# Kernel tuning notes

Hardware: AMD Instinct MI355X
Metric: run time of the kernel (lower is better)

The kernel has to match this reference:

```python
import jax, jax.numpy as jnp
import numpy as np

B, S, HID = 2, 2048, 2048
NH, NKV, HD = 16, 8, 256
EPS = 1e-6
SCALE = 256 ** -0.5  # query_pre_attn_scalar ** -0.5


def setup_inputs() -> dict:
    key = jax.random.key(0)
    k1, k2, k3 = jax.random.split(key, 3)
    hidden_states = jax.random.normal(k1, (B, S, HID), dtype=jnp.float32)
    w_qkv = jax.random.normal(k2, (HID, (NH + 2 * NKV) * HD), dtype=jnp.float32) * 0.02
    w_o = jax.random.normal(k3, (NH * HD, HID), dtype=jnp.float32) * 0.02
    q_norm_w = jnp.zeros((HD,), dtype=jnp.float32)  # Gemma RMSNorm uses (1 + w)
    k_norm_w = jnp.zeros((HD,), dtype=jnp.float32)
    # Real rotary tables: inv_freq over half dim, emb = concat(freqs, freqs)
    inv_freq = 1.0 / (10000.0 ** (jnp.arange(0, HD, 2, dtype=jnp.float32) / HD))
    pos = jnp.arange(S, dtype=jnp.float32)
    freqs = pos[:, None] * inv_freq[None, :]            # [S, HD/2]
    emb = jnp.concatenate([freqs, freqs], axis=-1)       # [S, HD]
    cos = jnp.broadcast_to(jnp.cos(emb)[None], (B, S, HD))
    sin = jnp.broadcast_to(jnp.sin(emb)[None], (B, S, HD))
    return {"hidden_states": hidden_states, "cos": cos, "sin": sin,
            "w_qkv": w_qkv, "w_o": w_o, "q_norm_w": q_norm_w, "k_norm_w": k_norm_w}


def _rms_norm(x, w):
    # Gemma3RMSNorm: fp32 rms, scale by (1 + w)
    xf = x.astype(jnp.float32)
    var = jnp.mean(xf * xf, axis=-1, keepdims=True)
    out = xf * jax.lax.rsqrt(var + EPS) * (1.0 + w.astype(jnp.float32))
    return out.astype(x.dtype)


def _rotate_half(x):
    x1, x2 = jnp.split(x, 2, axis=-1)
    return jnp.concatenate([-x2, x1], axis=-1)


def reference(hidden_states, cos, sin, w_qkv, w_o, q_norm_w, k_norm_w):
    qkv = jnp.einsum("bsh,hf->bsf", hidden_states, w_qkv)
    q, k, v = jnp.split(qkv, [NH * HD, NH * HD + NKV * HD], axis=-1)
    q = q.reshape(B, S, NH, HD).transpose(0, 2, 1, 3)    # [b, nh, s, d]
    k = k.reshape(B, S, NKV, HD).transpose(0, 2, 1, 3)   # [b, nkv, s, d]
    v = v.reshape(B, S, NKV, HD).transpose(0, 2, 1, 3)
    q = _rms_norm(q, q_norm_w)
    k = _rms_norm(k, k_norm_w)
    c = cos[:, None, :, :]  # broadcast over heads
    s = sin[:, None, :, :]
    q = q * c + _rotate_half(q) * s
    k = k * c + _rotate_half(k) * s
    n_rep = NH // NKV
    k = jnp.repeat(k, n_rep, axis=1)  # GQA expand: [b, nh, s, d]
    v = jnp.repeat(v, n_rep, axis=1)
    scores = jnp.einsum("bhqd,bhkd->bhqk", q, k) * SCALE
    attn = jax.nn.softmax(scores, axis=-1)
    out = jnp.einsum("bhqk,bhkd->bhqd", attn, v)
    out = out.transpose(0, 2, 1, 3).reshape(B, S, NH * HD)
    return jnp.einsum("bsf,fh->bsh", out, w_o)
```

## Files before the change

kernel.cpp:

```cpp
#include <hip/hip_runtime.h>
#include <stdint.h>

typedef __attribute__((ext_vector_type(8))) short short8;
typedef __attribute__((ext_vector_type(4))) short short4v;
typedef __attribute__((ext_vector_type(4))) float f32x4;

#define GLOAD16(gp, lp) __builtin_amdgcn_global_load_lds( \
    (__attribute__((address_space(1))) void*)(gp),        \
    (__attribute__((address_space(3))) void*)(lp), 16, 0, 0)

#define BAR   __builtin_amdgcn_s_barrier()
#define LGKM0 asm volatile("s_waitcnt lgkmcnt(0)" ::: "memory")
#define VMCNT4 asm volatile("s_waitcnt vmcnt(4)" ::: "memory")

__device__ __forceinline__ unsigned short f2bf(float f) {
    union { float f; unsigned u; } v; v.f = f;
    unsigned u = v.u + 0x7fffu + ((v.u >> 16) & 1u);
    return (unsigned short)(u >> 16);
}
__device__ __forceinline__ float bf2f(short s) {
    union { unsigned u; float f; } v;
    v.u = ((unsigned)(unsigned short)s) << 16;
    return v.f;
}

__global__ __launch_bounds__(256) void cvt_f32_bf16(const float* __restrict__ in,
                                                    short* __restrict__ out) {
    const int i = (blockIdx.x * 256 + threadIdx.x) * 4;
    const float4 v = *(const float4*)(in + i);
    short4v o;
    o[0] = (short)f2bf(v.x); o[1] = (short)f2bf(v.y);
    o[2] = (short)f2bf(v.z); o[3] = (short)f2bf(v.w);
    *(short4v*)(out + i) = o;
}

__global__ __launch_bounds__(256) void transpose_cvt(const float* __restrict__ in,
                                                     short* __restrict__ out,
                                                     int R, int C) {
    __shared__ float tile[64 * 65];
    const int t = threadIdx.x;
    const int r0 = blockIdx.y * 64, c0 = blockIdx.x * 64;
    const int rl = t >> 4, cl4 = (t & 15) * 4;
#pragma unroll
    for (int rep = 0; rep < 4; rep++) {
        const int r = rep * 16 + rl;
        const float4 v = *(const float4*)(in + (long)(r0 + r) * C + c0 + cl4);
        tile[r * 65 + cl4 + 0] = v.x;
        tile[r * 65 + cl4 + 1] = v.y;
        tile[r * 65 + cl4 + 2] = v.z;
        tile[r * 65 + cl4 + 3] = v.w;
    }
    __syncthreads();
#pragma unroll
    for (int rep = 0; rep < 4; rep++) {
        const int cc = rep * 16 + rl;
        short4v o;
#pragma unroll
        for (int j = 0; j < 4; j++) o[j] = (short)f2bf(tile[(cl4 + j) * 65 + cc]);
        *(short4v*)(out + (long)(c0 + cc) * R + r0 + cl4) = o;
    }
}

__global__ __launch_bounds__(256) void vtrans(const short* __restrict__ QKV,
                                              short* __restrict__ Vt) {
    __shared__ short tile[64 * 72];
    const int t = threadIdx.x;
    const int s0 = blockIdx.x * 64, d0 = blockIdx.y * 64;
    const int hb = blockIdx.z >> 1, b = blockIdx.z & 1;
    const short* src = QKV + ((long)(24 + hb) * 4096 + b * 2048) * 256;
    short* dst = Vt + (long)blockIdx.z * 256 * 2048;
#pragma unroll
    for (int p = 0; p < 2; p++) {
        const int c = p * 256 + t;
        const int r = c >> 3, col8 = (c & 7) * 8;
        *(short8*)(tile + r * 72 + col8) = *(const short8*)(src + (long)(s0 + r) * 256 + d0 + col8);
    }
    __syncthreads();
#pragma unroll
    for (int p = 0; p < 2; p++) {
        const int c = p * 256 + t;
        const int dr = c >> 3, sc8 = (c & 7) * 8;
        short8 o;
#pragma unroll
        for (int j = 0; j < 8; j++) o[j] = tile[(sc8 + j) * 72 + dr];
        *(short8*)(dst + (long)(d0 + dr) * 2048 + s0 + sc8) = o;
    }
}

template<int N, int K, int OUTMODE>
__global__ __launch_bounds__(256) void gemm_nt(const short* __restrict__ A,
                                               const short* __restrict__ Bt,
                                               void* __restrict__ Cv) {
    __shared__ __align__(16) short Al[128 * 32];
    __shared__ __align__(16) short Bl[128 * 32];
    const int t = threadIdx.x;
    const int lane = t & 63, w = t >> 6;
    const int quad = lane >> 4, l16 = lane & 15;
    const int wr = w >> 1, wc = w & 1;
    const long m0 = (long)blockIdx.y * 128, n0 = (long)blockIdx.x * 128;

    const short* Ag0 = A + (m0 + (t >> 2)) * K + (t & 3) * 8;
    const short* Bg0 = Bt + (n0 + (t >> 2)) * K + (t & 3) * 8;

    f32x4 acc[4][4] = {};

    for (int k0 = 0; k0 < K; k0 += 32) {
        __syncthreads();
        GLOAD16(Ag0 + k0,            Al + t * 8);
        GLOAD16(Ag0 + 64 * K + k0,   Al + (t + 256) * 8);
        GLOAD16(Bg0 + k0,            Bl + t * 8);
        GLOAD16(Bg0 + 64 * K + k0,   Bl + (t + 256) * 8);
        __syncthreads();
        short8 af[4], bfr[4];
#pragma unroll
        for (int i = 0; i < 4; i++)
            af[i] = *(const short8*)(Al + (wr * 64 + i * 16 + l16) * 32 + quad * 8);
#pragma unroll
        for (int i = 0; i < 4; i++)
            bfr[i] = *(const short8*)(Bl + (wc * 64 + i * 16 + l16) * 32 + quad * 8);
#pragma unroll
        for (int mi = 0; mi < 4; mi++)
#pragma unroll
            for (int ni = 0; ni < 4; ni++)
                acc[mi][ni] = __builtin_amdgcn_mfma_f32_16x16x32_bf16(af[mi], bfr[ni], acc[mi][ni], 0, 0, 0);
    }

    const long crow = m0 + wr * 64 + quad * 4;
    const long ccol = n0 + wc * 64 + l16;
    if constexpr (OUTMODE == 0) {
        float* C = (float*)Cv;
#pragma unroll
        for (int mi = 0; mi < 4; mi++)
#pragma unroll
            for (int ni = 0; ni < 4; ni++)
#pragma unroll
                for (int r = 0; r < 4; r++)
                    C[(crow + mi * 16 + r) * N + ccol + ni * 16] = acc[mi][ni][r];
    } else {
        short* C = (short*)Cv;
#pragma unroll
        for (int mi = 0; mi < 4; mi++)
#pragma unroll
            for (int ni = 0; ni < 4; ni++)
#pragma unroll
                for (int r = 0; r < 4; r++) {
                    const long m = crow + mi * 16 + r;
                    const long f = ccol + ni * 16;
                    C[(f >> 8) * 1048576 + m * 256 + (f & 255)] = (short)f2bf(acc[mi][ni][r]);
                }
    }
}

__global__ __launch_bounds__(512, 2) void gemm256_qkv(const short* __restrict__ A,
                                                      const short* __restrict__ Bt,
                                                      short* __restrict__ QKV) {
    constexpr int K = 2048;
    constexpr int NTM = 31;
    __shared__ __align__(16) short L[2][4][8192];

    const int t = threadIdx.x;
    const int lane = t & 63, w = t >> 6;
    const int quad = lane >> 4, l16 = lane & 15;
    const int wr = w >> 2, wc = w & 3;
    const int bh = 2 + (wc >> 1);
    const int brow0 = (wc & 1) * 64;

    const int flat = blockIdx.y * 32 + blockIdx.x;
    const int swz = (flat & 7) * 64 + (flat >> 3);
    const int bx = swz & 31, by = swz >> 5;
    const long m0 = (long)by * 256, n0 = (long)bx * 256;

    const int r0 = t >> 3, r1 = (512 + t) >> 3;
    const int k0s = ((t & 7) * 8) ^ (((r0 >> 2) & 1) << 4);
    const int k1s = ((t & 7) * 8) ^ (((r1 >> 2) & 1) << 4);
    const short* aS0 = A + (m0 + r0) * K + k0s;
    const short* aS1 = A + (m0 + r1) * K + k1s;
    const short* aT0 = aS0 + 128 * K;
    const short* aT1 = aS1 + 128 * K;
    const short* bS0 = Bt + (n0 + r0) * K + k0s;
    const short* bS1 = Bt + (n0 + r1) * K + k1s;
    const short* bT0 = bS0 + 128 * K;
    const short* bT1 = bS1 + 128 * K;

#define STG(p0, p1, bsel, slot, kt) do {                     \
    const int _ko = ((kt) & NTM) * 64;                       \
    GLOAD16((p0) + _ko, &L[bsel][slot][t * 8]);              \
    GLOAD16((p1) + _ko, &L[bsel][slot][4096 + t * 8]);       \
} while (0)

#define LDA4(bsel, rb) do {                                                        \
    _Pragma("unroll") for (int m = 0; m < 4; ++m) {                                \
        const int _r = (rb) + m * 16 + l16;                                        \
        const int _sw = ((_r >> 2) & 1) << 4;                                      \
        a[m][0] = *(const short8*)(&L[bsel][wr][_r * 64 + ((quad * 8) ^ _sw)]);    \
        a[m][1] = *(const short8*)(&L[bsel][wr][_r * 64 + ((32 + quad * 8) ^ _sw)]); \
    } } while (0)

#define LDB2(bsel, nb) do {                                                        \
    _Pragma("unroll") for (int n = 0; n < 2; ++n) {                                \
        const int _r = brow0 + ((nb) + n) * 16 + l16;                              \
        const int _sw = ((_r >> 2) & 1) << 4;                                      \
        b[(nb) + n][0] = *(const short8*)(&L[bsel][bh][_r * 64 + ((quad * 8) ^ _sw)]); \
        b[(nb) + n][1] = *(const short8*)(&L[bsel][bh][_r * 64 + ((32 + quad * 8) ^ _sw)]); \
    } } while (0)

#define PH_MFMA(MB, NB)                                                            \
    __builtin_amdgcn_s_setprio(1);                                                 \
    _Pragma("unroll") for (int m = 0; m < 4; ++m)                                  \
    _Pragma("unroll") for (int n = 0; n < 2; ++n)                                  \
    _Pragma("unroll") for (int kk = 0; kk < 2; ++kk)                               \
        acc[(MB) + m][(NB) + n] = __builtin_amdgcn_mfma_f32_16x16x32_bf16(         \
            a[m][kk], b[(NB) + n][kk], acc[(MB) + m][(NB) + n], 0, 0, 0);          \
    __builtin_amdgcn_s_setprio(0);

    short8 a[4][2], b[4][2];
    f32x4 acc[8][4] = {};

    STG(aS0, aS1, 0, 0, 0);
    STG(aT0, aT1, 0, 1, 0);
    STG(bS0, bS1, 0, 2, 0);
    STG(bT0, bT1, 0, 3, 0);
    STG(bS0, bS1, 1, 2, 1);
    STG(bT0, bT1, 1, 3, 1);
    VMCNT4;
    BAR;

    for (int it = 0; it < 16; ++it) {
        const int kt0 = 2 * it;
        LDA4(0, 0);
        LDB2(0, 0);
        STG(aS0, aS1, 1, 0, kt0 + 1);
        BAR; LGKM0;
        PH_MFMA(0, 0);
        BAR;
        LDB2(0, 2);
        STG(aT0, aT1, 1, 1, kt0 + 1);
        BAR; LGKM0;
        PH_MFMA(0, 2);
        BAR;
        LDA4(0, 64);
        STG(bS0, bS1, 0, 2, kt0 + 2);
        BAR; LGKM0;
        PH_MFMA(4, 2);
        BAR;
        STG(bT0, bT1, 0, 3, kt0 + 2);
        BAR;
        PH_MFMA(4, 0);
        VMCNT4;
        BAR;
        LDA4(1, 0);
        LDB2(1, 0);
        STG(aS0, aS1, 0, 0, kt0 + 2);
        BAR; LGKM0;
        PH_MFMA(0, 0);
        BAR;
        LDB2(1, 2);
        STG(aT0, aT1, 0, 1, kt0 + 2);
        BAR; LGKM0;
        PH_MFMA(0, 2);
        BAR;
        LDA4(1, 64);
        STG(bS0, bS1, 1, 2, kt0 + 3);
        BAR; LGKM0;
        PH_MFMA(4, 2);
        BAR;
        STG(bT0, bT1, 1, 3, kt0 + 3);
        BAR;
        PH_MFMA(4, 0);
        VMCNT4;
        BAR;
    }

    short* Cp = QKV + (long)bx * 1048576;
    const int cbase = wc * 64;
#pragma unroll
    for (int mi = 0; mi < 8; ++mi)
#pragma unroll
        for (int ni = 0; ni < 4; ++ni)
#pragma unroll
            for (int r = 0; r < 4; ++r) {
                const long m = m0 + wr * 128 + mi * 16 + quad * 4 + r;
                Cp[m * 256 + cbase + ni * 16 + l16] = (short)f2bf(acc[mi][ni][r]);
            }

#undef STG
#undef LDA4
#undef LDB2
#undef PH_MFMA
}

__global__ __launch_bounds__(256) void prep_qk(short* __restrict__ QKV,
                                               const float* __restrict__ cosp,
                                               const float* __restrict__ sinp,
                                               const float* __restrict__ qw,
                                               const float* __restrict__ kw) {
    const int t = threadIdx.x, w = t >> 6, lane = t & 63;
    const int d4 = lane * 4;
    const float sgn = (lane < 32) ? -1.0f : 1.0f;
#pragma unroll
    for (int i = 0; i < 4; i++) {
        const int g = blockIdx.x * 16 + w * 4 + i;
        const int u = g >> 12, m = g & 4095;
        short* rowp = QKV + (long)g * 256;
        const short4v raw = *(const short4v*)(rowp + d4);
        float x[4];
#pragma unroll
        for (int j = 0; j < 4; j++) x[j] = bf2f(raw[j]);
        float ss = x[0]*x[0] + x[1]*x[1] + x[2]*x[2] + x[3]*x[3];
#pragma unroll
        for (int msk = 1; msk < 64; msk <<= 1) ss += __shfl_xor(ss, msk, 64);
        const float rinv = rsqrtf(ss * (1.0f / 256.0f) + 1e-6f);
        const float4 wv = *(const float4*)(((u < 16) ? qw : kw) + d4);
        const float wa[4] = {wv.x, wv.y, wv.z, wv.w};
        const float4 cv = *(const float4*)(cosp + (long)m * 256 + d4);
        const float4 sv = *(const float4*)(sinp + (long)m * 256 + d4);
        const float ca[4] = {cv.x, cv.y, cv.z, cv.w};
        const float sa[4] = {sv.x, sv.y, sv.z, sv.w};
        float n[4];
#pragma unroll
        for (int j = 0; j < 4; j++) n[j] = x[j] * rinv * (1.0f + wa[j]);
        const float scale = (u < 16) ? 0.0625f : 1.0f;
        short4v ov;
#pragma unroll
        for (int j = 0; j < 4; j++) {
            const float p = __shfl_xor(n[j], 32, 64);
            ov[j] = (short)f2bf((n[j] * ca[j] + sgn * p * sa[j]) * scale);
        }
        *(short4v*)(rowp + d4) = ov;
    }
}

__global__ __launch_bounds__(512, 2) void attn(const short* __restrict__ QKV,
                                               const short* __restrict__ Vt,
                                               short* __restrict__ O) {
    __shared__ __align__(16) short Kl[2][64 * 256];
    __shared__ __align__(16) short Vl[256 * 64];
    __shared__ __align__(16) short Pl[128 * 72];
    __shared__ __align__(16) float Ll[128];

    const int t = threadIdx.x, w = t >> 6, lane = t & 63;
    const int quad = lane >> 4, l16 = lane & 15;
    const int q0 = blockIdx.x * 128, h = blockIdx.y, b = blockIdx.z;
    const int kh = h >> 1;
    const short* Qp = QKV + ((long)h * 4096 + b * 2048 + q0) * 256;
    const short* Kp = QKV + ((long)(16 + kh) * 4096 + b * 2048) * 256;
    const short* Vp = Vt + (long)(kh * 2 + b) * 256 * 2048;

    short8 qf[8];
#pragma unroll
    for (int ks = 0; ks < 8; ks++)
        qf[ks] = *(const short8*)(Qp + (w * 16 + l16) * 256 + ks * 32 + quad * 8);

    f32x4 acc[4][4] = {};
    float li_[4] = {0.0f, 0.0f, 0.0f, 0.0f};

    const int qh = w >> 2, dstr = (w & 3) * 64;

#pragma unroll
    for (int i = 0; i < 4; i++) {
        const int c = i * 512 + t;
        const int rK = c >> 5, j = c & 31;
        GLOAD16(Kp + (long)rK * 256 + (j ^ (rK & 31)) * 8, Kl[0] + c * 8);
    }

    for (int kt = 0; kt < 32; kt++) {
        const int k0 = kt * 64;
        __syncthreads();

#pragma unroll
        for (int i = 0; i < 4; i++) {
            const int c = i * 512 + t;
            const int dV = c >> 3, j = c & 7;
            GLOAD16(Vp + (long)dV * 2048 + k0 + (j ^ (dV & 7)) * 8, Vl + c * 8);
        }
        const int kn = ((kt + 1) & 31) * 64;
#pragma unroll
        for (int i = 0; i < 4; i++) {
            const int c = i * 512 + t;
            const int rK = c >> 5, j = c & 31;
            GLOAD16(Kp + (long)(kn + rK) * 256 + (j ^ (rK & 31)) * 8, Kl[(kt + 1) & 1] + c * 8);
        }

        const short* Kb = Kl[kt & 1];
        f32x4 sc[4] = {};
#pragma unroll
        for (int ct = 0; ct < 4; ct++) {
            const int rowK = ct * 16 + l16;
#pragma unroll
            for (int ks = 0; ks < 8; ks++) {
                const int dc = (ks * 4 + quad) ^ (rowK & 31);
                const short8 kf = *(const short8*)(Kb + rowK * 256 + dc * 8);
                sc[ct] = __builtin_amdgcn_mfma_f32_16x16x32_bf16(qf[ks], kf, sc[ct], 0, 0, 0);
            }
        }

#pragma unroll
        for (int ct = 0; ct < 4; ct++) {
#pragma unroll
            for (int r = 0; r < 4; r++) {
                const float p = __expf(sc[ct][r]);
                li_[r] += p;
                Pl[(w * 16 + quad * 4 + r) * 72 + ct * 16 + l16] = (short)f2bf(p);
            }
        }
        __syncthreads();

#pragma unroll
        for (int k2 = 0; k2 < 2; k2++) {
            short8 pf[4];
#pragma unroll
            for (int mi2 = 0; mi2 < 4; mi2++)
                pf[mi2] = *(const short8*)(Pl + (qh * 64 + mi2 * 16 + l16) * 72 + k2 * 32 + quad * 8);
#pragma unroll
            for (int ni = 0; ni < 4; ni++) {
                const int dV = dstr + ni * 16 + l16;
                const int dc = (k2 * 4 + quad) ^ (dV & 7);
                const short8 vf = *(const short8*)(Vl + dV * 64 + dc * 8);
#pragma unroll
                for (int mi2 = 0; mi2 < 4; mi2++)
                    acc[mi2][ni] = __builtin_amdgcn_mfma_f32_16x16x32_bf16(pf[mi2], vf, acc[mi2][ni], 0, 0, 0);
            }
        }
    }

#pragma unroll
    for (int r = 0; r < 4; r++) {
        float v = li_[r];
        v += __shfl_xor(v, 1, 64);
        v += __shfl_xor(v, 2, 64);
        v += __shfl_xor(v, 4, 64);
        v += __shfl_xor(v, 8, 64);
        if (l16 == 0) Ll[w * 16 + quad * 4 + r] = v;
    }
    __syncthreads();

    short* Op = O + (long)(b * 2048 + q0 + qh * 64) * 4096 + h * 256 + dstr;
#pragma unroll
    for (int mi2 = 0; mi2 < 4; mi2++) {
        const float4 lv = *(const float4*)(Ll + qh * 64 + mi2 * 16 + quad * 4);
        const float inv[4] = {1.0f / lv.x, 1.0f / lv.y, 1.0f / lv.z, 1.0f / lv.w};
#pragma unroll
        for (int ni = 0; ni < 4; ni++)
#pragma unroll
            for (int r = 0; r < 4; r++)
                Op[(long)(mi2 * 16 + quad * 4 + r) * 4096 + ni * 16 + l16] =
                    (short)f2bf(acc[mi2][ni][r] * inv[r]);
    }
}

extern "C" void kernel_launch(void* const* d_in, const int* in_sizes, int n_in,
                              void* d_out, int out_size, void* d_ws, size_t ws_size,
                              hipStream_t stream) {
    const float* hs   = (const float*)d_in[0];
    const float* cosp = (const float*)d_in[1];
    const float* sinp = (const float*)d_in[2];
    const float* wqkv = (const float*)d_in[3];
    const float* wo   = (const float*)d_in[4];
    const float* qnw  = (const float*)d_in[5];
    const float* knw  = (const float*)d_in[6];
    float* out = (float*)d_out;

    short* poolA  = (short*)d_ws;
    short* Xb     = poolA;
    short* Wqkv_t = poolA + (size_t)4096 * 2048;
    short* QKV    = poolA + (size_t)4096 * 2048 + (size_t)8192 * 2048;
    short* Vt     = poolA;
    short* Ob     = poolA + (size_t)16 * 256 * 2048;
    short* Wo_t   = QKV;

    cvt_f32_bf16<<<8192, 256, 0, stream>>>(hs, Xb);
    transpose_cvt<<<dim3(128, 32), 256, 0, stream>>>(wqkv, Wqkv_t, 2048, 8192);
    gemm256_qkv<<<dim3(32, 16), 512, 0, stream>>>(Xb, Wqkv_t, QKV);
    prep_qk<<<6144, 256, 0, stream>>>(QKV, cosp, sinp, qnw, knw);
    vtrans<<<dim3(32, 4, 16), 256, 0, stream>>>(QKV, Vt);
    attn<<<dim3(16, 16, 2), 512, 0, stream>>>(QKV, Vt, Ob);
    transpose_cvt<<<dim3(32, 64), 256, 0, stream>>>(wo, Wo_t, 4096, 2048);
    gemm_nt<2048, 4096, 0><<<dim3(16, 32), 256, 0, stream>>>(Ob, Wo_t, (void*)out);
}
```

Before: 608.3 us.

## Retile attention QK^T into 32x32 warp tiles with swizzled P buffer and priority hints

Each wave now computes a 32x32 block of scores, with two query sub-tiles sharing each K fragment, instead of 16x64. This halves the K LDS reads per MFMA. The P scratch buffer drops its padding in favour of an XOR swizzle, which saves LDS while avoiding bank conflicts. s_setprio is raised around the MFMA sections. Row sums are now split across two waves, so extra barriers are needed to combine them in LDS, and each wave holds twice the Q fragment registers.

```diff
diff --git a/kernel.cpp b/kernel.cpp
--- a/kernel.cpp
+++ b/kernel.cpp
@@ -335,7 +335,7 @@
                                                short* __restrict__ O) {
     __shared__ __align__(16) short Kl[2][64 * 256];
     __shared__ __align__(16) short Vl[256 * 64];
-    __shared__ __align__(16) short Pl[128 * 72];
+    __shared__ __align__(16) short Pl[128 * 64];
     __shared__ __align__(16) float Ll[128];
 
     const int t = threadIdx.x, w = t >> 6, lane = t & 63;
@@ -346,13 +346,16 @@
     const short* Kp = QKV + ((long)(16 + kh) * 4096 + b * 2048) * 256;
     const short* Vp = Vt + (long)(kh * 2 + b) * 256 * 2048;
 
-    short8 qf[8];
-#pragma unroll
-    for (int ks = 0; ks < 8; ks++)
-        qf[ks] = *(const short8*)(Qp + (w * 16 + l16) * 256 + ks * 32 + quad * 8);
+    const int qh2 = w >> 1, kh2 = w & 1;
+    short8 qf2[2][8];
+#pragma unroll
+    for (int mi = 0; mi < 2; mi++)
+#pragma unroll
+        for (int ks = 0; ks < 8; ks++)
+            qf2[mi][ks] = *(const short8*)(Qp + (qh2 * 32 + mi * 16 + l16) * 256 + ks * 32 + quad * 8);
 
     f32x4 acc[4][4] = {};
-    float li_[4] = {0.0f, 0.0f, 0.0f, 0.0f};
+    float li_[2][4] = {};
 
     const int qh = w >> 2, dstr = (w & 3) * 64;
 
@@ -382,35 +385,44 @@
         }
 
         const short* Kb = Kl[kt & 1];
-        f32x4 sc[4] = {};
-#pragma unroll
-        for (int ct = 0; ct < 4; ct++) {
-            const int rowK = ct * 16 + l16;
+        f32x4 sc[2][2] = {};
+        __builtin_amdgcn_s_setprio(1);
+#pragma unroll
+        for (int ct2 = 0; ct2 < 2; ct2++) {
+            const int rowK = kh2 * 32 + ct2 * 16 + l16;
 #pragma unroll
             for (int ks = 0; ks < 8; ks++) {
                 const int dc = (ks * 4 + quad) ^ (rowK & 31);
                 const short8 kf = *(const short8*)(Kb + rowK * 256 + dc * 8);
-                sc[ct] = __builtin_amdgcn_mfma_f32_16x16x32_bf16(qf[ks], kf, sc[ct], 0, 0, 0);
+                sc[0][ct2] = __builtin_amdgcn_mfma_f32_16x16x32_bf16(qf2[0][ks], kf, sc[0][ct2], 0, 0, 0);
+                sc[1][ct2] = __builtin_amdgcn_mfma_f32_16x16x32_bf16(qf2[1][ks], kf, sc[1][ct2], 0, 0, 0);
             }
         }
-
-#pragma unroll
-        for (int ct = 0; ct < 4; ct++) {
-#pragma unroll
-            for (int r = 0; r < 4; r++) {
-                const float p = __expf(sc[ct][r]);
-                li_[r] += p;
-                Pl[(w * 16 + quad * 4 + r) * 72 + ct * 16 + l16] = (short)f2bf(p);
-            }
-        }
+        __builtin_amdgcn_s_setprio(0);
+
+#pragma unroll
+        for (int mi = 0; mi < 2; mi++)
+#pragma unroll
+            for (int ct2 = 0; ct2 < 2; ct2++)
+#pragma unroll
+                for (int r = 0; r < 4; r++) {
+                    const float p = __expf(sc[mi][ct2][r]);
+                    li_[mi][r] += p;
+                    const int prow = qh2 * 32 + mi * 16 + quad * 4 + r;
+                    const int pcol = kh2 * 32 + ct2 * 16 + l16;
+                    Pl[prow * 64 + (pcol ^ ((prow & 7) << 3))] = (short)f2bf(p);
+                }
         __syncthreads();
 
+        __builtin_amdgcn_s_setprio(1);
 #pragma unroll
         for (int k2 = 0; k2 < 2; k2++) {
             short8 pf[4];
 #pragma unroll
-            for (int mi2 = 0; mi2 < 4; mi2++)
-                pf[mi2] = *(const short8*)(Pl + (qh * 64 + mi2 * 16 + l16) * 72 + k2 * 32 + quad * 8);
+            for (int mi2 = 0; mi2 < 4; mi2++) {
+                const int prow = qh * 64 + mi2 * 16 + l16;
+                pf[mi2] = *(const short8*)(Pl + prow * 64 + ((k2 * 32 + quad * 8) ^ ((prow & 7) << 3)));
+            }
 #pragma unroll
             for (int ni = 0; ni < 4; ni++) {
                 const int dV = dstr + ni * 16 + l16;
@@ -421,16 +433,36 @@
                     acc[mi2][ni] = __builtin_amdgcn_mfma_f32_16x16x32_bf16(pf[mi2], vf, acc[mi2][ni], 0, 0, 0);
             }
         }
-    }
-
-#pragma unroll
-    for (int r = 0; r < 4; r++) {
-        float v = li_[r];
-        v += __shfl_xor(v, 1, 64);
-        v += __shfl_xor(v, 2, 64);
-        v += __shfl_xor(v, 4, 64);
-        v += __shfl_xor(v, 8, 64);
-        if (l16 == 0) Ll[w * 16 + quad * 4 + r] = v;
+        __builtin_amdgcn_s_setprio(0);
+    }
+
+    float lv_[2][4];
+#pragma unroll
+    for (int mi = 0; mi < 2; mi++)
+#pragma unroll
+        for (int r = 0; r < 4; r++) {
+            float v = li_[mi][r];
+            v += __shfl_xor(v, 1, 64);
+            v += __shfl_xor(v, 2, 64);
+            v += __shfl_xor(v, 4, 64);
+            v += __shfl_xor(v, 8, 64);
+            lv_[mi][r] = v;
+        }
+    __syncthreads();
+    if (kh2 == 0 && l16 == 0) {
+#pragma unroll
+        for (int mi = 0; mi < 2; mi++)
+#pragma unroll
+            for (int r = 0; r < 4; r++)
+                Ll[qh2 * 32 + mi * 16 + quad * 4 + r] = lv_[mi][r];
+    }
+    __syncthreads();
+    if (kh2 == 1 && l16 == 0) {
+#pragma unroll
+        for (int mi = 0; mi < 2; mi++)
+#pragma unroll
+            for (int r = 0; r < 4; r++)
+                Ll[qh2 * 32 + mi * 16 + quad * 4 + r] += lv_[mi][r];
     }
     __syncthreads();
 
```

After: 585.5 us (median of 2 runs). -3.7%, faster.
